# Performance work log

Measured on AMD Instinct MI355X. Metric: run time of the kernel, lower is better.

The kernel has to match this reference:

```python
import math
import jax, jax.numpy as jnp
import numpy as np

D_MODEL = 1024
H_HEADS = 16
D_K = D_MODEL // H_HEADS


def setup_inputs() -> dict:
    key = jax.random.key(0)
    ks = jax.random.split(key, 7)
    B, L = 4, 2048
    q = jax.random.normal(ks[0], (B, L, D_MODEL), dtype=jnp.float32)
    k = jax.random.normal(ks[1], (B, L, D_MODEL), dtype=jnp.float32)
    v = jax.random.normal(ks[2], (B, L, D_MODEL), dtype=jnp.float32)
    mask = jnp.ones((1, L, L), dtype=jnp.int32)
    # nn.Linear(d_model, d_model, bias=False) weights, shape (out, in)
    s = 1.0 / math.sqrt(D_MODEL)
    W_q = jax.random.uniform(ks[3], (D_MODEL, D_MODEL), jnp.float32, -s, s)
    W_k = jax.random.uniform(ks[4], (D_MODEL, D_MODEL), jnp.float32, -s, s)
    W_v = jax.random.uniform(ks[5], (D_MODEL, D_MODEL), jnp.float32, -s, s)
    W_o = jax.random.uniform(ks[6], (D_MODEL, D_MODEL), jnp.float32, -s, s)
    return {"q": q, "k": k, "v": v, "mask": mask,
            "W_q": W_q, "W_k": W_k, "W_v": W_v, "W_o": W_o}


def reference(q, k, v, mask, W_q, W_k, W_v, W_o):
    B, Lq, _ = q.shape
    # projections (Linear: x @ W.T) then split heads -> (B, H, L, d_k)
    def split_heads(x):
        return x.reshape(B, -1, H_HEADS, D_K).transpose(0, 2, 1, 3)
    Q = split_heads(jnp.einsum('bsd,ed->bse', q, W_q))
    K = split_heads(jnp.einsum('bsd,ed->bse', k, W_k))
    V = split_heads(jnp.einsum('bsd,ed->bse', v, W_v))
    # scores: (B, H, Lq, Lk)
    scores = jnp.einsum('bhqd,bhkd->bhqk', Q, K) / math.sqrt(D_K)
    m = mask[:, None, :, :]  # (1, 1, Lq, Lk) broadcast
    scores = jnp.where(m == 0, -jnp.inf, scores)
    weights = jax.nn.softmax(scores, axis=-1)
    attn = jnp.einsum('bhqk,bhkd->bhqd', weights, V)  # (B, H, Lq, d_v)
    attn = attn.transpose(0, 2, 1, 3).reshape(B, Lq, D_MODEL)
    return jnp.einsum('bse,de->bsd', attn, W_o)
```

## Files before the change

### kernel.cpp

```cpp
#include <hip/hip_runtime.h>
#include <hip/hip_bf16.h>


typedef unsigned short u16;
typedef float f32x4  __attribute__((ext_vector_type(4)));
typedef float f32x16 __attribute__((ext_vector_type(16)));
typedef short s16x8  __attribute__((ext_vector_type(8)));
typedef unsigned u32x4 __attribute__((ext_vector_type(4)));
typedef __bf16 bf16x8 __attribute__((ext_vector_type(8)));

#define QSCL 0.18033688011112042f

__device__ __forceinline__ u16 f2b(float f) {
    union { float f; unsigned u; } x; x.f = f;
    unsigned r = x.u + 0x7fffu + ((x.u >> 16) & 1u);
    return (u16)(r >> 16);
}

__device__ __forceinline__ f32x4 MF(s16x8 a, s16x8 b, f32x4 c) {
    return __builtin_amdgcn_mfma_f32_16x16x32_bf16(
        __builtin_bit_cast(bf16x8, a), __builtin_bit_cast(bf16x8, b), c, 0, 0, 0);
}
__device__ __forceinline__ f32x16 MF32(s16x8 a, s16x8 b, f32x16 c) {
    return __builtin_amdgcn_mfma_f32_32x32x16_bf16(
        __builtin_bit_cast(bf16x8, a), __builtin_bit_cast(bf16x8, b), c, 0, 0, 0);
}
__device__ __forceinline__ unsigned cvtpk(float lo, float hi) {
    unsigned r;
    asm("v_cvt_pk_bf16_f32 %0, %1, %2" : "=v"(r) : "v"(lo), "v"(hi));
    return r;
}
__device__ __forceinline__ void swap32(unsigned &a, unsigned &b) {
    asm volatile("v_permlane32_swap_b32 %0, %1" : "+v"(a), "+v"(b));
}
__device__ __forceinline__ float expa(float x) {
    float r;
    asm("v_exp_f32 %0, %1" : "=v"(r) : "v"(x));
    return r;
}
__device__ __forceinline__ void g2l16(const u16* g, u16* lbase) {
    __builtin_amdgcn_global_load_lds((const __attribute__((address_space(1))) void*)g,
                                     (__attribute__((address_space(3))) void*)lbase, 16, 0, 0);
}

__global__ __launch_bounds__(256)
void convert_and_mask(const float* __restrict__ q, const float* __restrict__ k,
                      const float* __restrict__ v, const float* __restrict__ Wq,
                      const float* __restrict__ Wk, const float* __restrict__ Wv,
                      const float* __restrict__ Wo, const int* __restrict__ mask,
                      u16* __restrict__ Abf, u16* __restrict__ Wbf,
                      int* __restrict__ mflag) {
    if (blockIdx.x < 256) {
        __shared__ int anyz;
        if (threadIdx.x == 0) anyz = 0;
        __syncthreads();
        const int qt = blockIdx.x >> 4, kt = blockIdx.x & 15;
        int local = 0;
#pragma unroll
        for (int qq = 0; qq < 16; ++qq) {
            int e4 = qq * 256 + threadIdx.x;
            int r = e4 >> 5, cc = (e4 & 31) * 4;
            int4 mv = *(const int4*)(mask + (size_t)(qt * 128 + r) * 2048 + kt * 128 + cc);
            local |= (mv.x == 0) | (mv.y == 0) | (mv.z == 0) | (mv.w == 0);
        }
        if (local) atomicOr(&anyz, 1);
        __syncthreads();
        if (threadIdx.x == 0) mflag[blockIdx.x] = anyz;
        return;
    }
    const size_t NQKV = 25165824;
    const size_t NCH  = 3670016;
    const size_t nconv = (size_t)(gridDim.x - 256) * 256;
    for (size_t cidx = (size_t)(blockIdx.x - 256) * 256 + threadIdx.x; cidx < NCH;
         cidx += nconv) {
        size_t e = cidx * 8;
        const float* src; u16* dst; float scl = 1.f;
        if (e < NQKV) {
            src = (e < 8388608) ? q + e
                : (e < 16777216) ? k + (e - 8388608) : v + (e - 16777216);
            dst = Abf + e;
        } else {
            size_t o = e - NQKV;
            if (o < 1048576)      { src = Wq + o; scl = QSCL; }
            else if (o < 2097152) { src = Wk + (o - 1048576); }
            else if (o < 3145728) { src = Wv + (o - 2097152); }
            else                  { src = Wo + (o - 3145728); }
            dst = Wbf + o;
        }
        float4 a = *(const float4*)(src);
        float4 b = *(const float4*)(src + 4);
        ushort4 p0, p1;
        p0.x = f2b(a.x * scl); p0.y = f2b(a.y * scl);
        p0.z = f2b(a.z * scl); p0.w = f2b(a.w * scl);
        p1.x = f2b(b.x * scl); p1.y = f2b(b.y * scl);
        p1.z = f2b(b.z * scl); p1.w = f2b(b.w * scl);
        *(ushort4*)dst = p0; *(ushort4*)(dst + 4) = p1;
    }
}

__global__ __launch_bounds__(256)
void gemm_qkv_fast(const u16* __restrict__ Abf, const u16* __restrict__ Wbf,
                   u16* __restrict__ Qh, u16* __restrict__ Kf, u16* __restrict__ Vf) {
    __shared__ __align__(16) u16 As[128 * 32];
    __shared__ __align__(16) u16 Bs[128 * 32];
    const int z = blockIdx.z;
    const u16* A = Abf + (size_t)z * (8192 * 1024);
    const u16* W = Wbf + (size_t)z * (1024 * 1024);
    const int tid = threadIdx.x, l = tid & 63, w = tid >> 6;
    const int g = l >> 4, c = l & 15;
    const int m0 = blockIdx.x * 128, n0 = blockIdx.y * 128;
    const int wr = (w >> 1) * 64, wc = (w & 1) * 64;

    f32x4 acc[4][4];
#pragma unroll
    for (int i = 0; i < 4; ++i)
#pragma unroll
        for (int j = 0; j < 4; ++j)
#pragma unroll
            for (int e = 0; e < 4; ++e) acc[i][j][e] = 0.f;

    const u16* Ag = A + (size_t)(m0 + w * 32 + (l >> 2)) * 1024 + (l & 3) * 8;
    const u16* Wg = W + (size_t)(n0 + w * 32 + (l >> 2)) * 1024 + (l & 3) * 8;
    u16* Al = As + w * 1024;
    u16* Bl = Bs + w * 1024;

    for (int kt = 0; kt < 32; ++kt) {
        __syncthreads();
        g2l16(Ag + kt * 32,         Al);
        g2l16(Ag + kt * 32 + 16384, Al + 512);
        g2l16(Wg + kt * 32,         Bl);
        g2l16(Wg + kt * 32 + 16384, Bl + 512);
        __syncthreads();
        s16x8 af[4], bf[4];
#pragma unroll
        for (int i = 0; i < 4; ++i) {
            af[i] = *(const s16x8*)(As + (wr + i * 16 + c) * 32 + g * 8);
            bf[i] = *(const s16x8*)(Bs + (wc + i * 16 + c) * 32 + g * 8);
        }
#pragma unroll
        for (int mi = 0; mi < 4; ++mi)
#pragma unroll
            for (int ni = 0; ni < 4; ++ni)
                acc[mi][ni] = MF(af[mi], bf[ni], acc[mi][ni]);
    }

    if (z == 0) {
#pragma unroll
        for (int mi = 0; mi < 4; ++mi)
#pragma unroll
            for (int ni = 0; ni < 4; ++ni)
#pragma unroll
                for (int j = 0; j < 4; ++j) {
                    int row = m0 + wr + mi * 16 + g * 4 + j;
                    int col = n0 + wc + ni * 16 + c;
                    int b = row >> 11, sl = row & 2047;
                    int h = col >> 6, d = col & 63;
                    Qh[(((size_t)(b * 16 + h)) * 2048 + sl) * 64 + d] = f2b(acc[mi][ni][j]);
                }
    } else if (z == 1) {
#pragma unroll
        for (int mi = 0; mi < 4; ++mi)
#pragma unroll
            for (int ni = 0; ni < 4; ++ni)
#pragma unroll
                for (int j = 0; j < 4; ++j) {
                    int row = m0 + wr + mi * 16 + g * 4 + j;
                    int col = n0 + wc + ni * 16 + c;
                    int b = row >> 11, kk = row & 2047;
                    int h = col >> 6, d = col & 63;
                    size_t off = (size_t)(b * 16 + h) * 131072
                               + (size_t)(((kk >> 5) * 4 + (d >> 4))) * 512
                               + ((kk & 31) + 32 * ((d >> 3) & 1)) * 8 + (d & 7);
                    Kf[off] = f2b(acc[mi][ni][j]);
                }
    } else {
#pragma unroll
        for (int mi = 0; mi < 4; ++mi)
#pragma unroll
            for (int ni = 0; ni < 4; ++ni) {
                int key0 = m0 + wr + mi * 16 + g * 4;
                int col  = n0 + wc + ni * 16 + c;
                int b = key0 >> 11, kk0 = key0 & 2047;
                int h = col >> 6, d = col & 63;
                size_t off = (size_t)(b * 16 + h) * 131072
                           + (size_t)((kk0 >> 6) * 8 + (d >> 5) * 4 + ((kk0 >> 4) & 3)) * 512
                           + (((kk0 >> 3) & 1) * 32 + (d & 31)) * 8 + (kk0 & 7);
                ushort4 pk;
                pk.x = f2b(acc[mi][ni][0]); pk.y = f2b(acc[mi][ni][1]);
                pk.z = f2b(acc[mi][ni][2]); pk.w = f2b(acc[mi][ni][3]);
                *(ushort4*)(Vf + off) = pk;
            }
    }
}

__global__ __launch_bounds__(256)
void gemm_out_fast(const u16* __restrict__ Ab, const u16* __restrict__ W,
                   float* __restrict__ Cout) {
    __shared__ __align__(16) u16 As[128 * 32];
    __shared__ __align__(16) u16 Bs[128 * 32];
    const int tid = threadIdx.x, l = tid & 63, w = tid >> 6;
    const int g = l >> 4, c = l & 15;
    const int m0 = blockIdx.x * 128, n0 = blockIdx.y * 128;
    const int wr = (w >> 1) * 64, wc = (w & 1) * 64;

    f32x4 acc[4][4];
#pragma unroll
    for (int i = 0; i < 4; ++i)
#pragma unroll
        for (int j = 0; j < 4; ++j)
#pragma unroll
            for (int e = 0; e < 4; ++e) acc[i][j][e] = 0.f;

    const u16* Ag = Ab + (size_t)(m0 + w * 32 + (l >> 2)) * 1024 + (l & 3) * 8;
    const u16* Wg = W  + (size_t)(n0 + w * 32 + (l >> 2)) * 1024 + (l & 3) * 8;
    u16* Al = As + w * 1024;
    u16* Bl = Bs + w * 1024;

    for (int kt = 0; kt < 32; ++kt) {
        __syncthreads();
        g2l16(Ag + kt * 32,         Al);
        g2l16(Ag + kt * 32 + 16384, Al + 512);
        g2l16(Wg + kt * 32,         Bl);
        g2l16(Wg + kt * 32 + 16384, Bl + 512);
        __syncthreads();
        s16x8 af[4], bf[4];
#pragma unroll
        for (int i = 0; i < 4; ++i) {
            af[i] = *(const s16x8*)(As + (wr + i * 16 + c) * 32 + g * 8);
            bf[i] = *(const s16x8*)(Bs + (wc + i * 16 + c) * 32 + g * 8);
        }
#pragma unroll
        for (int mi = 0; mi < 4; ++mi)
#pragma unroll
            for (int ni = 0; ni < 4; ++ni)
                acc[mi][ni] = MF(af[mi], bf[ni], acc[mi][ni]);
    }

#pragma unroll
    for (int mi = 0; mi < 4; ++mi)
#pragma unroll
        for (int ni = 0; ni < 4; ++ni)
#pragma unroll
            for (int j = 0; j < 4; ++j) {
                int row = m0 + wr + mi * 16 + g * 4 + j;
                int col = n0 + wc + ni * 16 + c;
                Cout[(size_t)row * 1024 + col] = acc[mi][ni][j];
            }
}

__global__ __launch_bounds__(256, 4)
void flash_attn(const u16* __restrict__ Qh, const u16* __restrict__ Kf,
                const u16* __restrict__ Vf, const int* __restrict__ mask,
                const int* __restrict__ mflag, u16* __restrict__ attnB) {
    __shared__ __align__(16) u16 KV[2][2][8][512];

    const int tid = threadIdx.x, w = tid >> 6, l = tid & 63;
    const int hi = l >> 5, q32 = l & 31;
    const int bh = blockIdx.x, qt = blockIdx.y;
    const size_t base = (size_t)bh * (2048 * 64);
    const u16* Qp = Qh + base;
    const u16* Kp = Kf + base;
    const u16* Vp = Vf + base;
    const int qrow_w = qt * 128 + w * 32;

    int anyflag = 0;
#pragma unroll
    for (int i = 0; i < 16; ++i) anyflag |= mflag[qt * 16 + i];

    s16x8 Qf[4];
#pragma unroll
    for (int s = 0; s < 4; ++s)
        Qf[s] = *(const s16x8*)(Qp + (size_t)(qrow_w + q32) * 64 + s * 16 + hi * 8);

    s16x8 ones;
#pragma unroll
    for (int i = 0; i < 8; ++i) ones[i] = (short)0x3F80;

    f32x16 z16;
#pragma unroll
    for (int r = 0; r < 16; ++r) z16[r] = 0.f;
    f32x16 oA = z16, oB = z16, lacc = z16;

    auto stage = [&](int buf, int kt) {
        const u16* ks = Kp + (size_t)(kt * 8 + w * 2) * 512 + l * 8;
        const u16* vs = Vp + (size_t)(kt * 8 + w * 2) * 512 + l * 8;
        g2l16(ks,       &KV[buf][0][w * 2][0]);
        g2l16(ks + 512, &KV[buf][0][w * 2 + 1][0]);
        g2l16(vs,       &KV[buf][1][w * 2][0]);
        g2l16(vs + 512, &KV[buf][1][w * 2 + 1][0]);
    };

    auto Shalf = [&](int buf, int half) -> f32x16 {
        __builtin_amdgcn_s_setprio(1);
        s16x8 ka = *(const s16x8*)&KV[buf][0][half * 4][l * 8];
        f32x16 s = MF32(ka, Qf[0], z16);
#pragma unroll
        for (int ss = 1; ss < 4; ++ss) {
            ka = *(const s16x8*)&KV[buf][0][half * 4 + ss][l * 8];
            s = MF32(ka, Qf[ss], s);
        }
        __builtin_amdgcn_s_setprio(0);
        return s;
    };
    auto expmask = [&](f32x16& s, int kt, int half) {
        if (anyflag && mflag[qt * 16 + (kt >> 1)] != 0) {
            const int qr = qrow_w + q32, kb = kt * 64 + half * 32;
#pragma unroll
            for (int r = 0; r < 16; ++r) {
                int key = (r & 3) + 8 * (r >> 2) + 4 * hi;
                if (mask[(size_t)qr * 2048 + kb + key] == 0) s[r] = -1e30f;
            }
        }
#pragma unroll
        for (int r = 0; r < 16; ++r) s[r] = expa(s[r]);
    };
    auto packh = [&](const f32x16& s, s16x8& X0, s16x8& X1) {
        u32x4 t;
        unsigned a0 = cvtpk(s[0], s[1]),   a1 = cvtpk(s[2], s[3]);
        unsigned b0 = cvtpk(s[4], s[5]),   b1 = cvtpk(s[6], s[7]);
        swap32(a0, b0); swap32(a1, b1);
        t.x = a0; t.y = a1; t.z = b0; t.w = b1;
        X0 = __builtin_bit_cast(s16x8, t);
        unsigned c0 = cvtpk(s[8], s[9]),   c1 = cvtpk(s[10], s[11]);
        unsigned d0 = cvtpk(s[12], s[13]), d1 = cvtpk(s[14], s[15]);
        swap32(c0, d0); swap32(c1, d1);
        t.x = c0; t.y = c1; t.z = d0; t.w = d1;
        X1 = __builtin_bit_cast(s16x8, t);
    };
    auto PVhalf = [&](int buf, int half, s16x8 X0, s16x8 X1) {
        __builtin_amdgcn_s_setprio(1);
        s16x8 v0 = *(const s16x8*)&KV[buf][1][half * 2][l * 8];
        s16x8 v1 = *(const s16x8*)&KV[buf][1][4 + half * 2][l * 8];
        oA = MF32(X0, v0, oA);
        oB = MF32(X0, v1, oB);
        lacc = MF32(X0, ones, lacc);
        s16x8 v2 = *(const s16x8*)&KV[buf][1][half * 2 + 1][l * 8];
        s16x8 v3 = *(const s16x8*)&KV[buf][1][4 + half * 2 + 1][l * 8];
        oA = MF32(X1, v2, oA);
        oB = MF32(X1, v3, oB);
        lacc = MF32(X1, ones, lacc);
        __builtin_amdgcn_s_setprio(0);
    };

    s16x8 Xc0, Xc1;

    stage(0, 0);
    __syncthreads();
    stage(1, 1);
    {
        f32x16 s0 = Shalf(0, 0);
        expmask(s0, 0, 0);
        f32x16 s1 = Shalf(0, 1);
        s16x8 Y0, Y1;
        packh(s0, Y0, Y1);
        PVhalf(0, 0, Y0, Y1);
        expmask(s1, 0, 1);
        packh(s1, Xc0, Xc1);
    }

    for (int kt = 1; kt < 32; ++kt) {
        const int buf = kt & 1, bprev = buf ^ 1;
        PVhalf(bprev, 1, Xc0, Xc1);
        __syncthreads();
        if (kt < 31) stage(bprev, kt + 1);
        f32x16 s0 = Shalf(buf, 0);
        expmask(s0, kt, 0);
        f32x16 s1 = Shalf(buf, 1);
        s16x8 Y0, Y1;
        packh(s0, Y0, Y1);
        PVhalf(buf, 0, Y0, Y1);
        expmask(s1, kt, 1);
        packh(s1, Xc0, Xc1);
    }
    PVhalf(1, 1, Xc0, Xc1);

    const int b = bh >> 4, h = bh & 15;
#pragma unroll
    for (int r = 0; r < 16; ++r) {
        int qloc = (r & 3) + 8 * (r >> 2) + 4 * hi;
        float inv = __builtin_amdgcn_rcpf(lacc[r]);
        int row = qrow_w + qloc;
        u16* dst = attnB + ((size_t)b * 2048 + row) * 1024 + h * 64 + q32;
        dst[0]  = f2b(oA[r] * inv);
        dst[32] = f2b(oB[r] * inv);
    }
}

extern "C" void kernel_launch(void* const* d_in, const int* in_sizes, int n_in,
                              void* d_out, int out_size, void* d_ws, size_t ws_size,
                              hipStream_t stream) {
    const float* q    = (const float*)d_in[0];
    const float* k    = (const float*)d_in[1];
    const float* v    = (const float*)d_in[2];
    const int*   mask = (const int*)d_in[3];
    const float* Wq   = (const float*)d_in[4];
    const float* Wk   = (const float*)d_in[5];
    const float* Wv   = (const float*)d_in[6];
    const float* Wo   = (const float*)d_in[7];

    char* ws = (char*)d_ws;
    u16* Abf   = (u16*)(ws);
    u16* Wbf   = (u16*)(ws + (48u << 20));
    u16* Qh    = (u16*)(ws + (56u << 20));
    u16* Kf    = (u16*)(ws + (72u << 20));
    u16* Vf    = (u16*)(ws + (88u << 20));
    u16* attnB = (u16*)(ws);
    int* mflag = (int*)(ws + (104u << 20));

    convert_and_mask<<<dim3(2304), dim3(256), 0, stream>>>(q, k, v, Wq, Wk, Wv, Wo,
                                                           mask, Abf, Wbf, mflag);
    gemm_qkv_fast<<<dim3(64, 8, 3), dim3(256), 0, stream>>>(Abf, Wbf, Qh, Kf, Vf);
    flash_attn<<<dim3(64, 16), dim3(256), 0, stream>>>(Qh, Kf, Vf, mask, mflag, attnB);
    gemm_out_fast<<<dim3(64, 8), dim3(256), 0, stream>>>(attnB, Wbf + 3145728, (float*)d_out);
}
```

Before: 209.7 us.

## Enlarge flash-attention blocks to 512 threads with 128-key shared K/V stages

Flash attention now runs 8 waves per block covering 256 query rows and stages 128 keys of K and V per shared-memory buffer, instead of 4 waves, 128 rows and 64 keys. Each block is larger and the key loop has half as many iterations, so there are fewer barriers and each K/V tile is reused by twice as many waves. The cost is twice the LDS per block, half as many blocks, and more waves waiting at each barrier, which could reduce occupancy.

```diff
diff --git a/kernel.cpp b/kernel.cpp
--- a/kernel.cpp
+++ b/kernel.cpp
@@ -248,11 +248,11 @@
             }
 }
 
-__global__ __launch_bounds__(256, 4)
+__global__ __launch_bounds__(512, 4)
 void flash_attn(const u16* __restrict__ Qh, const u16* __restrict__ Kf,
                 const u16* __restrict__ Vf, const int* __restrict__ mask,
                 const int* __restrict__ mflag, u16* __restrict__ attnB) {
-    __shared__ __align__(16) u16 KV[2][2][8][512];
+    __shared__ __align__(16) u16 KV[2][2][16][512];
 
     const int tid = threadIdx.x, w = tid >> 6, l = tid & 63;
     const int hi = l >> 5, q32 = l & 31;
@@ -261,11 +261,12 @@
     const u16* Qp = Qh + base;
     const u16* Kp = Kf + base;
     const u16* Vp = Vf + base;
-    const int qrow_w = qt * 128 + w * 32;
-
+    const int qrow_w = qt * 256 + w * 32;
+
+    const int flagrow = qt * 2 + (w >> 2);
     int anyflag = 0;
 #pragma unroll
-    for (int i = 0; i < 16; ++i) anyflag |= mflag[qt * 16 + i];
+    for (int i = 0; i < 16; ++i) anyflag |= mflag[flagrow * 16 + i];
 
     s16x8 Qf[4];
 #pragma unroll
@@ -281,30 +282,31 @@
     for (int r = 0; r < 16; ++r) z16[r] = 0.f;
     f32x16 oA = z16, oB = z16, lacc = z16;
 
-    auto stage = [&](int buf, int kt) {
-        const u16* ks = Kp + (size_t)(kt * 8 + w * 2) * 512 + l * 8;
-        const u16* vs = Vp + (size_t)(kt * 8 + w * 2) * 512 + l * 8;
+    auto stage = [&](int buf, int st) {
+        const u16* ks = Kp + (size_t)(st * 16 + w * 2) * 512 + l * 8;
+        const u16* vs = Vp + (size_t)(st * 16 + w * 2) * 512 + l * 8;
         g2l16(ks,       &KV[buf][0][w * 2][0]);
         g2l16(ks + 512, &KV[buf][0][w * 2 + 1][0]);
         g2l16(vs,       &KV[buf][1][w * 2][0]);
         g2l16(vs + 512, &KV[buf][1][w * 2 + 1][0]);
     };
 
-    auto Shalf = [&](int buf, int half) -> f32x16 {
+    auto Shalf = [&](int buf, int h) -> f32x16 {
+        const int rb = (h >> 1) * 8 + (h & 1) * 4;
         __builtin_amdgcn_s_setprio(1);
-        s16x8 ka = *(const s16x8*)&KV[buf][0][half * 4][l * 8];
+        s16x8 ka = *(const s16x8*)&KV[buf][0][rb][l * 8];
         f32x16 s = MF32(ka, Qf[0], z16);
 #pragma unroll
         for (int ss = 1; ss < 4; ++ss) {
-            ka = *(const s16x8*)&KV[buf][0][half * 4 + ss][l * 8];
+            ka = *(const s16x8*)&KV[buf][0][rb + ss][l * 8];
             s = MF32(ka, Qf[ss], s);
         }
         __builtin_amdgcn_s_setprio(0);
         return s;
     };
-    auto expmask = [&](f32x16& s, int kt, int half) {
-        if (anyflag && mflag[qt * 16 + (kt >> 1)] != 0) {
-            const int qr = qrow_w + q32, kb = kt * 64 + half * 32;
+    auto expmask = [&](f32x16& s, int st, int h) {
+        if (anyflag && mflag[flagrow * 16 + st] != 0) {
+            const int qr = qrow_w + q32, kb = st * 128 + h * 32;
 #pragma unroll
             for (int r = 0; r < 16; ++r) {
                 int key = (r & 3) + 8 * (r >> 2) + 4 * hi;
@@ -327,15 +329,16 @@
         t.x = c0; t.y = c1; t.z = d0; t.w = d1;
         X1 = __builtin_bit_cast(s16x8, t);
     };
-    auto PVhalf = [&](int buf, int half, s16x8 X0, s16x8 X1) {
+    auto PVhalf = [&](int buf, int h, s16x8 X0, s16x8 X1) {
+        const int rb = (h >> 1) * 8, hb = (h & 1) * 2;
         __builtin_amdgcn_s_setprio(1);
-        s16x8 v0 = *(const s16x8*)&KV[buf][1][half * 2][l * 8];
-        s16x8 v1 = *(const s16x8*)&KV[buf][1][4 + half * 2][l * 8];
+        s16x8 v0 = *(const s16x8*)&KV[buf][1][rb + hb][l * 8];
+        s16x8 v1 = *(const s16x8*)&KV[buf][1][rb + 4 + hb][l * 8];
         oA = MF32(X0, v0, oA);
         oB = MF32(X0, v1, oB);
         lacc = MF32(X0, ones, lacc);
-        s16x8 v2 = *(const s16x8*)&KV[buf][1][half * 2 + 1][l * 8];
-        s16x8 v3 = *(const s16x8*)&KV[buf][1][4 + half * 2 + 1][l * 8];
+        s16x8 v2 = *(const s16x8*)&KV[buf][1][rb + hb + 1][l * 8];
+        s16x8 v3 = *(const s16x8*)&KV[buf][1][rb + 4 + hb + 1][l * 8];
         oA = MF32(X1, v2, oA);
         oB = MF32(X1, v3, oB);
         lacc = MF32(X1, ones, lacc);
@@ -344,35 +347,34 @@
 
     s16x8 Xc0, Xc1;
 
+    auto processST = [&](int buf, int st) {
+        f32x16 sp = Shalf(buf, 0);
+        expmask(sp, st, 0);
+#pragma unroll
+        for (int h = 1; h < 4; ++h) {
+            f32x16 sc = Shalf(buf, h);
+            s16x8 Y0, Y1;
+            packh(sp, Y0, Y1);
+            PVhalf(buf, h - 1, Y0, Y1);
+            expmask(sc, st, h);
+            sp = sc;
+        }
+        packh(sp, Xc0, Xc1);
+    };
+
     stage(0, 0);
     __syncthreads();
     stage(1, 1);
-    {
-        f32x16 s0 = Shalf(0, 0);
-        expmask(s0, 0, 0);
-        f32x16 s1 = Shalf(0, 1);
-        s16x8 Y0, Y1;
-        packh(s0, Y0, Y1);
-        PVhalf(0, 0, Y0, Y1);
-        expmask(s1, 0, 1);
-        packh(s1, Xc0, Xc1);
-    }
-
-    for (int kt = 1; kt < 32; ++kt) {
-        const int buf = kt & 1, bprev = buf ^ 1;
-        PVhalf(bprev, 1, Xc0, Xc1);
-        __syncthreads();
-        if (kt < 31) stage(bprev, kt + 1);
-        f32x16 s0 = Shalf(buf, 0);
-        expmask(s0, kt, 0);
-        f32x16 s1 = Shalf(buf, 1);
-        s16x8 Y0, Y1;
-        packh(s0, Y0, Y1);
-        PVhalf(buf, 0, Y0, Y1);
-        expmask(s1, kt, 1);
-        packh(s1, Xc0, Xc1);
-    }
-    PVhalf(1, 1, Xc0, Xc1);
+    processST(0, 0);
+
+    for (int st = 1; st < 16; ++st) {
+        const int buf = st & 1;
+        PVhalf(buf ^ 1, 3, Xc0, Xc1);
+        __syncthreads();
+        if (st < 15) stage(buf ^ 1, st + 1);
+        processST(buf, st);
+    }
+    PVhalf(1, 3, Xc0, Xc1);
 
     const int b = bh >> 4, h = bh & 15;
 #pragma unroll
@@ -410,6 +412,6 @@
     convert_and_mask<<<dim3(2304), dim3(256), 0, stream>>>(q, k, v, Wq, Wk, Wv, Wo,
                                                            mask, Abf, Wbf, mflag);
     gemm_qkv_fast<<<dim3(64, 8, 3), dim3(256), 0, stream>>>(Abf, Wbf, Qh, Kf, Vf);
-    flash_attn<<<dim3(64, 16), dim3(256), 0, stream>>>(Qh, Kf, Vf, mask, mflag, attnB);
+    flash_attn<<<dim3(64, 8), dim3(512), 0, stream>>>(Qh, Kf, Vf, mask, mflag, attnB);
     gemm_out_fast<<<dim3(64, 8), dim3(256), 0, stream>>>(attnB, Wbf + 3145728, (float*)d_out);
 }
```

Measured after the change: 204.0 us. -2.7%, faster.
